# Kernel optimization log

Hardware: AMD Instinct MI355X
Metric: run time of the kernel (lower is better)

## Reference

```python
import jax, jax.numpy as jnp
from jax import lax
import numpy as np

N, M, P, K = 2, 16384, 5023, 4
C_PLANE, HP = 32, 256
OUT_DIM = 32


def _harmonic(x):
    # pytorch3d HarmonicEmbedding(n=4, logspace, omega_0=1, append_input=True)
    f = jnp.asarray([1.0, 2.0, 4.0, 8.0], x.dtype)
    e = (x[..., None] * f).reshape(x.shape[:-1] + (-1,))  # [..., 12]
    return jnp.concatenate([jnp.sin(e), jnp.cos(e), x], axis=-1)  # [..., 27]


def _grid_sample2d(img, grid):
    # img [C,H,W], grid [M,2] (x->W, y->H) in [-1,1]; bilinear, zero pad, align_corners=False
    C, H, W = img.shape
    x = (grid[:, 0] + 1.0) * (W / 2.0) - 0.5
    y = (grid[:, 1] + 1.0) * (H / 2.0) - 0.5
    x0 = jnp.floor(x); y0 = jnp.floor(y)
    x1 = x0 + 1.0; y1 = y0 + 1.0
    wx1 = x - x0; wx0 = 1.0 - wx1
    wy1 = y - y0; wy0 = 1.0 - wy1
    def gather(ix, iy):
        valid = ((ix >= 0) & (ix < W) & (iy >= 0) & (iy < H)).astype(img.dtype)
        ixc = jnp.clip(ix, 0, W - 1).astype(jnp.int32)
        iyc = jnp.clip(iy, 0, H - 1).astype(jnp.int32)
        return img[:, iyc, ixc] * valid[None, :]  # [C,M]
    out = (gather(x0, y0) * (wx0 * wy0) + gather(x1, y0) * (wx1 * wy0)
           + gather(x0, y1) * (wx0 * wy1) + gather(x1, y1) * (wx1 * wy1))
    return out.T  # [M,C]


def _forward(coordinates, directions, points_position, tex_tplanes, emb_table,
             pw1, pb1, pw2, pb2, fw1, fb1, fw2, fb2, fw3, fb3, dw, db, rw1, rb1, rw2, rb2):
    c = coordinates
    p = points_position
    # --- triplane sampling (EG3D projections (x,y),(x,z),(z,x)), mean over planes ---
    proj = jnp.stack([c[..., :2],
                      c[..., jnp.array([0, 2])],
                      c[..., jnp.array([2, 0])]], axis=1)  # [N,3,M,2]
    tex = jax.vmap(jax.vmap(_grid_sample2d))(tex_tplanes, proj).mean(axis=1)  # [N,M,32]
    # --- KNN (squared distances, ascending, as pytorch3d knn_points) ---
    d2 = (jnp.sum(c * c, -1)[:, :, None] + jnp.sum(p * p, -1)[:, None, :]
          - 2.0 * jnp.einsum('nmc,npc->nmp', c, p))  # [N,M,P]
    negd, idx = lax.top_k(-d2, K)
    dist = -negd  # [N,M,K]
    nn = jax.vmap(lambda pts, i: pts[i])(p, idx)  # [N,M,K,3]
    pf = emb_table[idx]  # [N,M,K,32]
    rel = c[:, :, None, :] - nn
    rel = rel / jnp.maximum(jnp.linalg.norm(rel, axis=-1, keepdims=True), 1e-12)
    h = jnp.concatenate([pf, _harmonic(rel)], axis=-1)  # [N,M,K,59]
    h = jax.nn.relu(h @ pw1 + pb1) @ pw2 + pb2  # [N,M,K,32]
    w = 1.0 / dist
    w = w / jnp.sum(w, axis=1, keepdims=True)  # dim=1 exactly as in source
    pts_feat = jnp.sum(h * w[..., None], axis=2)  # [N,M,32]
    # --- dense MLP stack ---
    feat = jnp.concatenate([tex, pts_feat], axis=-1)  # [N,M,64]
    feat = jax.nn.relu(feat @ fw1 + fb1)
    feat = jax.nn.relu(feat @ fw2 + fb2)
    feat = feat @ fw3 + fb3  # [N,M,128]
    selector = jnp.all((c > -1.0) & (c < 1.0), axis=-1)  # [N,M]
    raw = (jax.nn.softplus(10.0 * (feat @ dw + db)) / 10.0) * selector[..., None]
    densities = 1.0 - jnp.exp(-raw)
    rays = directions / jnp.maximum(jnp.linalg.norm(directions, axis=-1, keepdims=True), 1e-12)
    rgb = jnp.concatenate([feat, _harmonic(rays)], axis=-1)  # [N,M,155]
    rgb = jax.nn.relu(rgb @ rw1 + rb1) @ rw2 + rb2  # [N,M,OUT_DIM]
    rgb = jnp.concatenate([jax.nn.sigmoid(rgb[..., :3]) * (1.0 + 2 * 0.001) - 0.001,
                           rgb[..., 3:]], axis=-1)
    return densities, rgb, dist


def setup_inputs() -> dict:
    key = jax.random.key(0)
    ks = jax.random.split(key, 16)
    rn = lambda k, s, sc=1.0: jax.random.normal(k, s, jnp.float32) * sc
    def lin(k, i, o):
        k1, k2 = jax.random.split(k)
        return rn(k1, (i, o), 1.0 / np.sqrt(i)), rn(k2, (o,), 0.01)
    coordinates = jax.random.uniform(ks[0], (N, M, 3), jnp.float32)
    directions = rn(ks[1], (N, M, 3))
    points_position = jax.random.uniform(ks[2], (N, P, 3), jnp.float32)
    tex_tplanes = rn(ks[3], (N, 3, C_PLANE, HP, HP))
    emb_table = rn(ks[4], (P, 32), 0.02)
    pw1, pb1 = lin(ks[5], 32 + 27, 64)
    pw2, pb2 = lin(ks[6], 64, 32)
    fw1, fb1 = lin(ks[7], 64, 128)
    fw2, fb2 = lin(ks[8], 128, 128)
    fw3, fb3 = lin(ks[9], 128, 128)
    dw, db = lin(ks[10], 128, 1)
    rw1, rb1 = lin(ks[11], 128 + 27, 64)
    rw2, rb2 = lin(ks[12], 64, OUT_DIM)
    return dict(coordinates=coordinates, directions=directions, points_position=points_position,
                tex_tplanes=tex_tplanes, emb_table=emb_table, pw1=pw1, pb1=pb1, pw2=pw2, pb2=pb2,
                fw1=fw1, fb1=fb1, fw2=fw2, fb2=fb2, fw3=fw3, fb3=fb3, dw=dw, db=db,
                rw1=rw1, rb1=rb1, rw2=rw2, rb2=rb2)


def reference(coordinates, directions, points_position, tex_tplanes, emb_table,
              pw1, pb1, pw2, pb2, fw1, fb1, fw2, fb2, fw3, fb3, dw, db, rw1, rb1, rw2, rb2):
    return _forward(coordinates, directions, points_position, tex_tplanes, emb_table,
                    pw1, pb1, pw2, pb2, fw1, fb1, fw2, fb2, fw3, fb3, dw, db, rw1, rb1, rw2, rb2)
```

## Files before the change

### kernel.cpp

```cpp
#include <hip/hip_runtime.h>
#include <float.h>
#include <math.h>

#define NB 2
#define MQ 16384
#define NQ (NB*MQ)
#define PP 5023
#define KNN 4
#define HPX 256
#define HWSZ (HPX*HPX)
#define GD 12
#define GC (GD*GD*GD)
#define CAND_MAX 1024

#define OUT_RGB_OFF  ((size_t)NQ)
#define OUT_DIST_OFF ((size_t)NQ + (size_t)NQ*32)

#define WS_SUMS_OFF   ((size_t)0x80000)
#define WS_PCNT_OFF   ((size_t)0x81000)
#define WS_PSTART_OFF ((size_t)0x85000)
#define WS_PCUR_OFF   ((size_t)0x89000)
#define WS_QCNT_OFF   ((size_t)0x8D000)
#define WS_QSTART_OFF ((size_t)0x91000)
#define WS_QCUR_OFF   ((size_t)0x95000)
#define WS_QID_OFF    ((size_t)0x99000)
#define WS_PG_OFF     ((size_t)0xC0000)
#define WS_PID_OFF    ((size_t)0xF0000)
#define WS_WP_OFF     ((size_t)0x100000)
#define WS_TEX_OFF    ((size_t)0x120000)

#define WP_PW1 0
#define WP_PW2 1920
#define WP_FW1 2944
#define WP_FW2 7040
#define WP_FW3 15232
#define WP_DW  23424
#define WP_RW1 23488
#define WP_RW2 28480

typedef __attribute__((ext_vector_type(2))) _Float16 half2v;

static __device__ __forceinline__ unsigned int pk2(float a, float b) {
    half2v h; h[0] = (_Float16)a; h[1] = (_Float16)b;
    return __builtin_bit_cast(unsigned int, h);
}
static __device__ __forceinline__ float2 upk(unsigned int u) {
    half2v h = __builtin_bit_cast(half2v, u);
    return make_float2((float)h[0], (float)h[1]);
}
static __device__ __forceinline__ float dot2(unsigned int a, unsigned int b, float c) {
    return __builtin_amdgcn_fdot2(__builtin_bit_cast(half2v, a),
                                  __builtin_bit_cast(half2v, b), c, false);
}
static __device__ __forceinline__ int cell_of(float x) {
    int g = (int)(x * (float)GD);
    return (g < 0) ? 0 : ((g > GD-1) ? GD-1 : g);
}

struct FusedArgs {
    const float* src[8];
    int off[8]; int din[8]; int dout[8];
};
__global__ __launch_bounds__(256) void k_fused(
    FusedArgs a, unsigned int* __restrict__ wp,
    const float* __restrict__ tex, unsigned int* __restrict__ tex16,
    const float* __restrict__ pts, const float* __restrict__ coords,
    unsigned int* __restrict__ pcnt, unsigned int* __restrict__ qcnt,
    int use_t)
{
    const int b = blockIdx.x;
    const int tid = threadIdx.x;
    if (b < 1536) {
        if (!use_t) return;
        const int n3 = b >> 8;
        const int hw = ((b & 255) << 8) + tid;
        const float* s = tex + (size_t)n3 * 32 * HWSZ + hw;
        float v[32];
#pragma unroll
        for (int c = 0; c < 32; ++c) v[c] = s[(size_t)c * HWSZ];
        uint4* d = (uint4*)(tex16 + ((size_t)n3 * HWSZ + hw) * 16);
#pragma unroll
        for (int c = 0; c < 4; ++c)
            d[c] = make_uint4(pk2(v[8*c], v[8*c+1]), pk2(v[8*c+2], v[8*c+3]),
                              pk2(v[8*c+4], v[8*c+5]), pk2(v[8*c+6], v[8*c+7]));
    } else if (b < 1536 + 256) {
        const int b2 = b - 1536;
        const int mid = b2 >> 5;
        const int idx = (b2 & 31) * 256 + tid;
        const int DIN = a.din[mid], DOUT = a.dout[mid];
        const int din2 = (DIN + 1) >> 1;
        if (idx >= din2 * DOUT) return;
        const int i2 = idx / DOUT, j = idx - i2 * DOUT;
        const float* s = a.src[mid];
        const float lo = s[(2*i2) * DOUT + j];
        const float hi = (2*i2 + 1 < DIN) ? s[(2*i2 + 1) * DOUT + j] : 0.f;
        wp[a.off[mid] + idx] = pk2(lo, hi);
    } else {
        const int i = (b - 1792) * 256 + tid;
        if (i < NB * PP) {
            const int n = (i >= PP) ? 1 : 0;
            const float px = pts[3*i], py = pts[3*i+1], pz = pts[3*i+2];
            const int c = (cell_of(pz)*GD + cell_of(py))*GD + cell_of(px);
            atomicAdd(&pcnt[n*GC + c], 1u);
        } else if (i - NB*PP < NQ) {
            const int q = i - NB*PP;
            const int n = q >> 14;
            const float cx = coords[3*q], cy = coords[3*q+1], cz = coords[3*q+2];
            const int c = (cell_of(cz)*GD + cell_of(cy))*GD + cell_of(cx);
            atomicAdd(&qcnt[n*GC + c], 1u);
        }
    }
}

__global__ __launch_bounds__(1024) void k_scan2(const unsigned int* __restrict__ pcnt,
                                                unsigned int* __restrict__ psta,
                                                unsigned int* __restrict__ pcur,
                                                const unsigned int* __restrict__ qcnt,
                                                unsigned int* __restrict__ qsta,
                                                unsigned int* __restrict__ qcur) {
    __shared__ unsigned int sc[1024];
    const int t = threadIdx.x;
#pragma unroll 1
    for (int which = 0; which < 2; ++which) {
        const unsigned int* cnt = which ? qcnt : pcnt;
        unsigned int* start  = which ? qsta : psta;
        unsigned int* cursor = which ? qcur : pcur;
        const int stride = which ? MQ : PP;
#pragma unroll 1
        for (int n = 0; n < 2; ++n) {
            const unsigned int* c = cnt + n*GC;
            unsigned int a = (2*t   < GC) ? c[2*t]   : 0u;
            unsigned int b = (2*t+1 < GC) ? c[2*t+1] : 0u;
            unsigned int s = a + b;
            sc[t] = s;
            __syncthreads();
            for (int off = 1; off < 1024; off <<= 1) {
                unsigned int v = (t >= off) ? sc[t - off] : 0u;
                __syncthreads();
                sc[t] += v;
                __syncthreads();
            }
            unsigned int excl = sc[t] - s;
            unsigned int base = n * stride;
            if (2*t < GC)   { start[n*GC + 2*t]   = base + excl;
                              cursor[n*GC + 2*t]  = base + excl; }
            if (2*t+1 < GC) { start[n*GC + 2*t+1] = base + excl + a;
                              cursor[n*GC + 2*t+1]= base + excl + a; }
            __syncthreads();
        }
    }
}

__global__ __launch_bounds__(256) void k_scatter(const float* __restrict__ pts,
                                                 const float* __restrict__ coords,
                                                 unsigned int* __restrict__ pcur,
                                                 unsigned int* __restrict__ qcur,
                                                 float4* __restrict__ pg,
                                                 int* __restrict__ pid,
                                                 int* __restrict__ qid) {
    const int i = blockIdx.x * 256 + threadIdx.x;
    if (i < NB * PP) {
        const int n = (i >= PP) ? 1 : 0;
        const int local = i - n * PP;
        const float px = pts[3*i], py = pts[3*i+1], pz = pts[3*i+2];
        const int c = (cell_of(pz)*GD + cell_of(py))*GD + cell_of(px);
        const unsigned int pos = atomicAdd(&pcur[n*GC + c], 1u);
        pg[pos] = make_float4(px, py, pz, fmaf(px, px, fmaf(py, py, pz*pz)));
        pid[pos] = local;
    } else if (i - NB*PP < NQ) {
        const int q = i - NB*PP;
        const int n = q >> 14;
        const float cx = coords[3*q], cy = coords[3*q+1], cz = coords[3*q+2];
        const int c = (cell_of(cz)*GD + cell_of(cy))*GD + cell_of(cx);
        const unsigned int pos = atomicAdd(&qcur[n*GC + c], 1u);
        qid[pos] = q;
    }
}

__global__ __launch_bounds__(256) void k_knn_cell(
    const float* __restrict__ coords,
    const unsigned int* __restrict__ pstart, const unsigned int* __restrict__ pcnt,
    const float4* __restrict__ pg, const int* __restrict__ pid,
    const unsigned int* __restrict__ qstart, const unsigned int* __restrict__ qcnt,
    const int* __restrict__ qid,
    float* __restrict__ odist, int* __restrict__ oidx)
{
    __shared__ float4 cand[CAND_MAX];
    __shared__ int    cidx[CAND_MAX];
    __shared__ unsigned int rs[25], ro[26];
    const int tid = threadIdx.x;
    const int bid = blockIdx.x;
    const int n = bid / GC, c = bid % GC;
    const unsigned int qn = qcnt[n*GC + c];
    if (qn == 0) return;
    const int gz = c / (GD*GD), gy = (c / GD) % GD, gx = c % GD;

    const int x0 = max(gx-2,0), x1 = min(gx+2,GD-1);
    const int y0 = max(gy-2,0), y1 = min(gy+2,GD-1), ny = y1-y0+1;
    const int z0 = max(gz-2,0), z1 = min(gz+2,GD-1), nz = z1-z0+1;
    const int nrow = ny*nz;

    __shared__ unsigned int rcnt[25];
    if (tid < nrow) {
        const int yy = y0 + tid % ny;
        const int zz = z0 + tid / ny;
        const int c0 = n*GC + (zz*GD + yy)*GD + x0;
        const int c1 = n*GC + (zz*GD + yy)*GD + x1;
        const unsigned int s = pstart[c0];
        rs[tid]   = s;
        rcnt[tid] = (pstart[c1] + pcnt[c1]) - s;
    }
    __syncthreads();
    if (tid == 0) {
        unsigned int acc = 0; ro[0] = 0;
        for (int t = 0; t < nrow; ++t) { acc += rcnt[t]; ro[t+1] = acc; }
    }
    __syncthreads();
    const unsigned int total = ro[nrow];
    const bool ovf = (total > CAND_MAX);
    if (!ovf) {
        for (unsigned int i = tid; i < total; i += 256) {
            int lo = 0, hi = nrow;
            while (hi - lo > 1) { int mid = (lo + hi) >> 1; if (ro[mid] <= i) lo = mid; else hi = mid; }
            const unsigned int src = rs[lo] + (i - ro[lo]);
            cand[i] = pg[src];
            cidx[i] = pid[src];
        }
    }
    __syncthreads();

    const float w = 1.0f / (float)GD;
    const float thresh = 4.f * w * w * 0.999f;
    const int grp = tid >> 4, l16 = tid & 15;
    const unsigned int qs = qstart[n*GC + c];

#define INS4(d, i) { \
        bool L3 = ((d) < bd3) || ((d) == bd3 && (i) < bi3); \
        bool L2 = ((d) < bd2) || ((d) == bd2 && (i) < bi2); \
        bool L1 = ((d) < bd1) || ((d) == bd1 && (i) < bi1); \
        bool L0 = ((d) < bd0) || ((d) == bd0 && (i) < bi0); \
        bd3 = L3 ? (L2 ? bd2 : (d)) : bd3;  bi3 = L3 ? (L2 ? bi2 : (i)) : bi3; \
        bd2 = L2 ? (L1 ? bd1 : (d)) : bd2;  bi2 = L2 ? (L1 ? bi1 : (i)) : bi2; \
        bd1 = L1 ? (L0 ? bd0 : (d)) : bd1;  bi1 = L1 ? (L0 ? bi0 : (i)) : bi1; \
        bd0 = L0 ? (d) : bd0;               bi0 = L0 ? (i) : bi0; }

#define MERGE16() { \
        float bd[4] = { bd0, bd1, bd2, bd3 }; \
        int   bi[4] = { bi0, bi1, bi2, bi3 }; \
        for (int mask = 1; mask < 16; mask <<= 1) { \
            float od[4]; int oi[4]; \
            for (int j = 0; j < 4; ++j) { od[j] = __shfl_xor(bd[j], mask); \
                                          oi[j] = __shfl_xor(bi[j], mask); } \
            float e[4]; int ei[4]; \
            for (int j = 0; j < 4; ++j) { \
                float ad = bd[j], xd = od[3-j]; \
                int   ai = bi[j], xi = oi[3-j]; \
                bool ta = (ad < xd) || (ad == xd && ai < xi); \
                e[j] = ta ? ad : xd; ei[j] = ta ? ai : xi; \
            } \
            { bool sw = (e[2] < e[0]) || (e[2] == e[0] && ei[2] < ei[0]); \
              if (sw) { float td=e[0]; e[0]=e[2]; e[2]=td; int ti=ei[0]; ei[0]=ei[2]; ei[2]=ti; } } \
            { bool sw = (e[3] < e[1]) || (e[3] == e[1] && ei[3] < ei[1]); \
              if (sw) { float td=e[1]; e[1]=e[3]; e[3]=td; int ti=ei[1]; ei[1]=ei[3]; ei[3]=ti; } } \
            { bool sw = (e[1] < e[0]) || (e[1] == e[0] && ei[1] < ei[0]); \
              if (sw) { float td=e[0]; e[0]=e[1]; e[1]=td; int ti=ei[0]; ei[0]=ei[1]; ei[1]=ti; } } \
            { bool sw = (e[3] < e[2]) || (e[3] == e[2] && ei[3] < ei[2]); \
              if (sw) { float td=e[2]; e[2]=e[3]; e[3]=td; int ti=ei[2]; ei[2]=ei[3]; ei[3]=ti; } } \
            for (int j = 0; j < 4; ++j) { bd[j] = e[j]; bi[j] = ei[j]; } \
        } \
        bd0 = bd[0]; bd1 = bd[1]; bd2 = bd[2]; bd3 = bd[3]; \
        bi0 = bi[0]; bi1 = bi[1]; bi2 = bi[2]; bi3 = bi[3]; }

#pragma unroll 1
    for (unsigned int qb = 0; qb < qn; qb += 16) {
        const unsigned int qi = qb + grp;
        if (qi >= qn) continue;
        const int q = qid[qs + qi];
        const float cx = coords[3*q], cy = coords[3*q+1], cz = coords[3*q+2];
        const float ccq = fmaf(cx, cx, fmaf(cy, cy, cz*cz));

        float bd0 = FLT_MAX, bd1 = FLT_MAX, bd2 = FLT_MAX, bd3 = FLT_MAX;
        int   bi0 = 0x7fffffff, bi1 = 0x7fffffff, bi2 = 0x7fffffff, bi3 = 0x7fffffff;

        if (!ovf) {
#pragma unroll 1
            for (unsigned int j = l16; j < total; j += 16) {
                const float4 P = cand[j];
                const int i = cidx[j];
                const float dt = fmaf(cx, P.x, fmaf(cy, P.y, cz * P.z));
                const float d = fmaf(-2.0f, dt, ccq + P.w);
                INS4(d, i)
            }
            MERGE16()
        }
        if (ovf || !(bd3 < thresh)) {
            bd0 = bd1 = bd2 = bd3 = FLT_MAX;
            bi0 = bi1 = bi2 = bi3 = 0x7fffffff;
#pragma unroll 1
            for (int j = l16; j < PP; j += 16) {
                const float4 P = pg[n*PP + j];
                const int i = pid[n*PP + j];
                const float dt = fmaf(cx, P.x, fmaf(cy, P.y, cz * P.z));
                const float d = fmaf(-2.0f, dt, ccq + P.w);
                INS4(d, i)
            }
            MERGE16()
        }
        if (l16 == 0) {
            *(float4*)(odist + (size_t)q*4) = make_float4(bd0, bd1, bd2, bd3);
            *(int4*)(oidx + (size_t)q*4)    = make_int4(bi0, bi1, bi2, bi3);
        }
    }
#undef INS4
#undef MERGE16
}

__global__ __launch_bounds__(1024) void k_sums(const float* __restrict__ dist,
                                               float* __restrict__ sums) {
    const int b = blockIdx.x;
    const int n = b >> 2, k = b & 3;
    float s = 0.f;
    for (int m = threadIdx.x; m < MQ; m += 1024)
        s += 1.0f / dist[((size_t)n * MQ + m) * 4 + k];
    __shared__ float red[1024];
    red[threadIdx.x] = s;
    __syncthreads();
    for (int off = 512; off > 0; off >>= 1) {
        if (threadIdx.x < off) red[threadIdx.x] += red[threadIdx.x + off];
        __syncthreads();
    }
    if (threadIdx.x == 0) sums[b] = red[0];
}

static __device__ __forceinline__ float harm_val(int h, float rx, float ry, float rz) {
    if (h >= 27) return 0.f;
    float v;
    if (h < 24) {
        int base = (h < 12) ? h : (h - 12);
        float rv = (base >> 2) == 0 ? rx : ((base >> 2) == 1 ? ry : rz);
        float e = rv * (float)(1 << (base & 3));
        v = (h < 12) ? sinf(e) : cosf(e);
    } else {
        v = (h == 24) ? rx : ((h == 25) ? ry : rz);
    }
    return v;
}

#define SW 128

template<int DIN2, int DOUT, int TILE>
__device__ __forceinline__ void gemv2(const unsigned int* Xp, int lane,
                                      const unsigned int* Wl,
                                      const float* __restrict__ bias, int j0,
                                      float (&aa)[TILE], float (&ab)[TILE]) {
    static_assert(TILE % 4 == 0, "");
#pragma unroll
    for (int u = 0; u < TILE; ++u) { aa[u] = bias[j0 + u]; ab[u] = aa[u]; }
#pragma unroll
    for (int i2 = 0; i2 < DIN2; ++i2) {
        const uint2 xv = *(const uint2*)(Xp + i2 * SW + 2*lane);
        const uint4* wr = (const uint4*)(Wl + i2 * DOUT + j0);
#pragma unroll
        for (int t = 0; t < TILE/4; ++t) {
            const uint4 w4 = wr[t];
            aa[4*t+0] = dot2(xv.x, w4.x, aa[4*t+0]);  ab[4*t+0] = dot2(xv.y, w4.x, ab[4*t+0]);
            aa[4*t+1] = dot2(xv.x, w4.y, aa[4*t+1]);  ab[4*t+1] = dot2(xv.y, w4.y, ab[4*t+1]);
            aa[4*t+2] = dot2(xv.x, w4.z, aa[4*t+2]);  ab[4*t+2] = dot2(xv.y, w4.z, ab[4*t+2]);
            aa[4*t+3] = dot2(xv.x, w4.w, aa[4*t+3]);  ab[4*t+3] = dot2(xv.y, w4.w, ab[4*t+3]);
        }
    }
}

__global__ __launch_bounds__(1024, 1) void k_main(
    const float* __restrict__ coords, const float* __restrict__ dirs,
    const float* __restrict__ pts, const float* __restrict__ tex_raw,
    const unsigned int* __restrict__ tex16, const float* __restrict__ emb,
    const unsigned int* __restrict__ wp,
    const float* __restrict__ pb1, const float* __restrict__ pb2,
    const float* __restrict__ fb1, const float* __restrict__ fb2,
    const float* __restrict__ fb3, const float* __restrict__ db,
    const float* __restrict__ rb1, const float* __restrict__ rb2,
    const int* __restrict__ idxbuf, const float* __restrict__ distbuf,
    const float* __restrict__ sums, float* __restrict__ out, int use_tex_t)
{
    __shared__ unsigned int S[128 * SW];
    __shared__ __align__(16) unsigned int W[16384];
    __shared__ float Rstg[128 * 33];
    const int tid  = threadIdx.x;
    const int lane = tid & 63;
    const int wv   = __builtin_amdgcn_readfirstlane(tid >> 6);
    const int q0   = blockIdx.x * 128;
    const int n    = q0 >> 14;
    const int qa   = q0 + 2*lane;

#define STAGE(dstu4, srcoff, len) { \
        const uint4* s4_ = (const uint4*)(wp + (srcoff)); \
        for (int i_ = tid; i_ < (len)/4; i_ += 1024) ((uint4*)W)[(dstu4) + i_] = s4_[i_]; }

    auto gatherA = [&](int kk) {
#pragma unroll
        for (int s = 0; s < 2; ++s) {
            const int q = qa + s;
            const int id = idxbuf[(size_t)q*4 + kk];
            if (wv < 8) {
                const float4 e = *(const float4*)(emb + (size_t)id * 32 + wv*4);
                S[(64 + 2*wv    )*SW + 2*lane + s] = pk2(e.x, e.y);
                S[(64 + 2*wv + 1)*SW + 2*lane + s] = pk2(e.z, e.w);
            } else {
                const int w8 = wv - 8;
                if (w8 < 7) {
                    const float cx = coords[q*3+0], cy = coords[q*3+1], cz = coords[q*3+2];
                    const float nx = pts[((size_t)n*PP + id)*3 + 0];
                    const float ny = pts[((size_t)n*PP + id)*3 + 1];
                    const float nz = pts[((size_t)n*PP + id)*3 + 2];
                    float rx = cx - nx, ry = cy - ny, rz = cz - nz;
                    float nrm = sqrtf(fmaf(rx, rx, fmaf(ry, ry, rz*rz)));
                    float inv = 1.f / fmaxf(nrm, 1e-12f);
                    rx *= inv; ry *= inv; rz *= inv;
#pragma unroll
                    for (int t = 0; t < 2; ++t) {
                        const int pr = 2*w8 + t;
                        S[(80 + pr)*SW + 2*lane + s] =
                            pk2(harm_val(2*pr, rx, ry, rz), harm_val(2*pr + 1, rx, ry, rz));
                    }
                }
            }
        }
    };

    unsigned int tex_pack[2];
    {
        const int g = wv;
#pragma unroll
        for (int s = 0; s < 2; ++s) {
            const int q = qa + s;
            const float cx = coords[q*3+0], cy = coords[q*3+1], cz = coords[q*3+2];
            float a0 = 0.f, a1 = 0.f;
#pragma unroll
            for (int pl = 0; pl < 3; ++pl) {
                float gx = (pl == 2) ? cz : cx;
                float gy = (pl == 0) ? cy : ((pl == 1) ? cz : cx);
                float x = (gx + 1.f) * 128.f - 0.5f;
                float y = (gy + 1.f) * 128.f - 0.5f;
                float x0f = floorf(x), y0f = floorf(y);
                float wx1 = x - x0f, wy1 = y - y0f;
                float wx0 = 1.f - wx1, wy0 = 1.f - wy1;
                int x0 = (int)x0f, y0 = (int)y0f;
                int n3 = n * 3 + pl;
                int  xs[4] = { x0, x0+1, x0,   x0+1 };
                int  ys[4] = { y0, y0,   y0+1, y0+1 };
                float wt[4] = { wx0*wy0, wx1*wy0, wx0*wy1, wx1*wy1 };
#pragma unroll
                for (int c = 0; c < 4; ++c) {
                    int xi = xs[c], yi = ys[c];
                    if (xi >= 0 && xi < HPX && yi >= 0 && yi < HPX) {
                        float wgt = wt[c];
                        if (use_tex_t) {
                            const unsigned int v = tex16[
                                ((size_t)n3 * HWSZ + (size_t)yi * HPX + xi) * 16 + g];
                            const float2 f = upk(v);
                            a0 = fmaf(wgt, f.x, a0);
                            a1 = fmaf(wgt, f.y, a1);
                        } else {
                            size_t base = ((size_t)(n3 * 32 + g * 2)) * HWSZ + (size_t)yi * HPX + xi;
                            a0 = fmaf(wgt, tex_raw[base], a0);
                            a1 = fmaf(wgt, tex_raw[base + HWSZ], a1);
                        }
                    }
                }
            }
            tex_pack[s] = pk2(a0 * (1.f/3.f), a1 * (1.f/3.f));
        }
    }

    STAGE(0,    WP_PW1, 1920)
    STAGE(512,  WP_PW2, 1024)
    STAGE(1024, WP_FW1, 4096)
    gatherA(0);
    __syncthreads();

    STAGE(2048, WP_FW2, 8192)

#pragma unroll 1
    for (int k = 0; k < KNN; ++k) {
        {
            float aa[4], ab[4];
            gemv2<30, 64, 4>(S + 64*SW, lane, W, pb1, wv * 4, aa, ab);
            S[(96 + 2*wv    )*SW + 2*lane + 0] = pk2(fmaxf(aa[0], 0.f), fmaxf(aa[1], 0.f));
            S[(96 + 2*wv    )*SW + 2*lane + 1] = pk2(fmaxf(ab[0], 0.f), fmaxf(ab[1], 0.f));
            S[(96 + 2*wv + 1)*SW + 2*lane + 0] = pk2(fmaxf(aa[2], 0.f), fmaxf(aa[3], 0.f));
            S[(96 + 2*wv + 1)*SW + 2*lane + 1] = pk2(fmaxf(ab[2], 0.f), fmaxf(ab[3], 0.f));
        }
        __syncthreads();
        {
            float aa[2], ab[2];
            aa[0] = pb2[wv*2 + 0]; aa[1] = pb2[wv*2 + 1];
            ab[0] = aa[0]; ab[1] = aa[1];
#pragma unroll
            for (int i2 = 0; i2 < 32; ++i2) {
                const uint2 xv = *(const uint2*)(S + (96 + i2)*SW + 2*lane);
                const unsigned int w0 = W[2048 + i2*32 + wv*2 + 0];
                const unsigned int w1 = W[2048 + i2*32 + wv*2 + 1];
                aa[0] = dot2(xv.x, w0, aa[0]);  ab[0] = dot2(xv.y, w0, ab[0]);
                aa[1] = dot2(xv.x, w1, aa[1]);  ab[1] = dot2(xv.y, w1, ab[1]);
            }
            const float da  = distbuf[(size_t)qa*4 + k];
            const float dbq = distbuf[(size_t)(qa+1)*4 + k];
            const float wka = (1.0f / da)  / sums[n*4 + k];
            const float wkb = (1.0f / dbq) / sums[n*4 + k];
            S[(k*16 + wv)*SW + 2*lane + 0] = pk2(wka * aa[0], wka * aa[1]);
            S[(k*16 + wv)*SW + 2*lane + 1] = pk2(wkb * ab[0], wkb * ab[1]);
        }
        if (k < KNN-1) {
            gatherA(k+1);
        } else {
            S[(64 + wv)*SW + 2*lane + 0] = tex_pack[0];
            S[(64 + wv)*SW + 2*lane + 1] = tex_pack[1];
#pragma unroll
            for (int s = 0; s < 2; ++s) {
                float a = 0.f, b = 0.f;
#pragma unroll
                for (int kk = 0; kk < 4; ++kk) {
                    float2 v = upk(S[(kk*16 + wv)*SW + 2*lane + s]);
                    a += v.x; b += v.y;
                }
                S[(80 + wv)*SW + 2*lane + s] = pk2(a, b);
            }
        }
        __syncthreads();
    }

    {
        float aa[8], ab[8];
        gemv2<32, 128, 8>(S + 64*SW, lane, W + 4096, fb1, wv * 8, aa, ab);
#pragma unroll
        for (int u = 0; u < 4; ++u) {
            S[(4*wv + u)*SW + 2*lane + 0] = pk2(fmaxf(aa[2*u], 0.f), fmaxf(aa[2*u+1], 0.f));
            S[(4*wv + u)*SW + 2*lane + 1] = pk2(fmaxf(ab[2*u], 0.f), fmaxf(ab[2*u+1], 0.f));
        }
    }
    __syncthreads();
    {
        float aa[8], ab[8];
        gemv2<64, 128, 8>(S, lane, W + 8192, fb2, wv * 8, aa, ab);
#pragma unroll
        for (int u = 0; u < 4; ++u) {
            S[(64 + 4*wv + u)*SW + 2*lane + 0] = pk2(fmaxf(aa[2*u], 0.f), fmaxf(aa[2*u+1], 0.f));
            S[(64 + 4*wv + u)*SW + 2*lane + 1] = pk2(fmaxf(ab[2*u], 0.f), fmaxf(ab[2*u+1], 0.f));
        }
    }
    STAGE(0, WP_FW3, 8192)
    __syncthreads();
    {
        float aa[8], ab[8];
        gemv2<64, 128, 8>(S + 64*SW, lane, W, fb3, wv * 8, aa, ab);
#pragma unroll
        for (int u = 0; u < 4; ++u) {
            S[(4*wv + u)*SW + 2*lane + 0] = pk2(aa[2*u], aa[2*u+1]);
            S[(4*wv + u)*SW + 2*lane + 1] = pk2(ab[2*u], ab[2*u+1]);
        }
    }
    STAGE(2048, WP_RW1, 4992)
    STAGE(3296, WP_RW2, 1024)
    STAGE(3552, WP_DW, 64)
    __syncthreads();
    if (wv < 14) {
#pragma unroll
        for (int s = 0; s < 2; ++s) {
            const int q = qa + s;
            float dx = dirs[q*3+0], dy = dirs[q*3+1], dz = dirs[q*3+2];
            float dn = sqrtf(fmaf(dx, dx, fmaf(dy, dy, dz*dz)));
            float inv = 1.f / fmaxf(dn, 1e-12f);
            dx *= inv; dy *= inv; dz *= inv;
            S[(64 + wv)*SW + 2*lane + s] = pk2(harm_val(2*wv, dx, dy, dz),
                                               harm_val(2*wv + 1, dx, dy, dz));
        }
    }
    __syncthreads();
    {
        float aa[4], ab[4];
        gemv2<78, 64, 4>(S, lane, W + 8192, rb1, wv * 4, aa, ab);
        S[(78 + 2*wv    )*SW + 2*lane + 0] = pk2(fmaxf(aa[0], 0.f), fmaxf(aa[1], 0.f));
        S[(78 + 2*wv    )*SW + 2*lane + 1] = pk2(fmaxf(ab[0], 0.f), fmaxf(ab[1], 0.f));
        S[(78 + 2*wv + 1)*SW + 2*lane + 0] = pk2(fmaxf(aa[2], 0.f), fmaxf(aa[3], 0.f));
        S[(78 + 2*wv + 1)*SW + 2*lane + 1] = pk2(fmaxf(ab[2], 0.f), fmaxf(ab[3], 0.f));
    }
    __syncthreads();
    {
        float aa[2], ab[2];
        aa[0] = rb2[wv*2 + 0]; aa[1] = rb2[wv*2 + 1];
        ab[0] = aa[0]; ab[1] = aa[1];
#pragma unroll
        for (int i2 = 0; i2 < 32; ++i2) {
            const uint2 xv = *(const uint2*)(S + (78 + i2)*SW + 2*lane);
            const unsigned int w0 = W[13184 + i2*32 + wv*2 + 0];
            const unsigned int w1 = W[13184 + i2*32 + wv*2 + 1];
            aa[0] = dot2(xv.x, w0, aa[0]);  ab[0] = dot2(xv.y, w0, ab[0]);
            aa[1] = dot2(xv.x, w1, aa[1]);  ab[1] = dot2(xv.y, w1, ab[1]);
        }
#pragma unroll
        for (int u = 0; u < 2; ++u) {
            const int j = wv*2 + u;
            float va = (u == 0) ? aa[0] : aa[1];
            float vb = (u == 0) ? ab[0] : ab[1];
            if (j < 3) {
                va = 1.002f * (1.f / (1.f + expf(-va))) - 0.001f;
                vb = 1.002f * (1.f / (1.f + expf(-vb))) - 0.001f;
            }
            Rstg[(2*lane    ) * 33 + j] = va;
            Rstg[(2*lane + 1) * 33 + j] = vb;
        }
        if (wv == 15) {
            float za = db[0], zb = db[0];
#pragma unroll 8
            for (int i2 = 0; i2 < 64; ++i2) {
                const uint2 xv = *(const uint2*)(S + i2*SW + 2*lane);
                const unsigned int wz = W[14208 + i2];
                za = dot2(xv.x, wz, za);
                zb = dot2(xv.y, wz, zb);
            }
#pragma unroll
            for (int s = 0; s < 2; ++s) {
                const int q = qa + s;
                const float z = (s == 0) ? za : zb;
                const float cx = coords[q*3+0], cy = coords[q*3+1], cz = coords[q*3+2];
                float selv = (cx > -1.f && cx < 1.f && cy > -1.f && cy < 1.f &&
                              cz > -1.f && cz < 1.f) ? 1.f : 0.f;
                float t10 = 10.f * z;
                float sp = (t10 > 20.f) ? t10 : log1pf(expf(t10));
                float raw = sp * 0.1f * selv;
                out[q] = 1.f - expf(-raw);
            }
        }
    }
    __syncthreads();
    {
        const int cq = tid >> 3;
        const int j0 = (tid & 7) * 4;
        float4 v;
        v.x = Rstg[cq*33 + j0 + 0];
        v.y = Rstg[cq*33 + j0 + 1];
        v.z = Rstg[cq*33 + j0 + 2];
        v.w = Rstg[cq*33 + j0 + 3];
        *(float4*)(out + OUT_RGB_OFF + ((size_t)(q0 + cq))*32 + j0) = v;
    }
#undef STAGE
}

extern "C" void kernel_launch(void* const* d_in, const int* in_sizes, int n_in,
                              void* d_out, int out_size, void* d_ws, size_t ws_size,
                              hipStream_t stream) {
    (void)in_sizes; (void)n_in; (void)out_size;
    const float* coords = (const float*)d_in[0];
    const float* dirs   = (const float*)d_in[1];
    const float* pts    = (const float*)d_in[2];
    const float* tex    = (const float*)d_in[3];
    const float* emb    = (const float*)d_in[4];
    const float* pw1 = (const float*)d_in[5];  const float* pb1 = (const float*)d_in[6];
    const float* pw2 = (const float*)d_in[7];  const float* pb2 = (const float*)d_in[8];
    const float* fw1 = (const float*)d_in[9];  const float* fb1 = (const float*)d_in[10];
    const float* fw2 = (const float*)d_in[11]; const float* fb2 = (const float*)d_in[12];
    const float* fw3 = (const float*)d_in[13]; const float* fb3 = (const float*)d_in[14];
    const float* dw  = (const float*)d_in[15]; const float* db  = (const float*)d_in[16];
    const float* rw1 = (const float*)d_in[17]; const float* rb1 = (const float*)d_in[18];
    const float* rw2 = (const float*)d_in[19]; const float* rb2 = (const float*)d_in[20];

    float*        out     = (float*)d_out;
    int*          wsidx   = (int*)d_ws;
    float*        wssums  = (float*)((char*)d_ws + WS_SUMS_OFF);
    unsigned int* wspcnt  = (unsigned int*)((char*)d_ws + WS_PCNT_OFF);
    unsigned int* wspsta  = (unsigned int*)((char*)d_ws + WS_PSTART_OFF);
    unsigned int* wspcur  = (unsigned int*)((char*)d_ws + WS_PCUR_OFF);
    unsigned int* wsqcnt  = (unsigned int*)((char*)d_ws + WS_QCNT_OFF);
    unsigned int* wsqsta  = (unsigned int*)((char*)d_ws + WS_QSTART_OFF);
    unsigned int* wsqcur  = (unsigned int*)((char*)d_ws + WS_QCUR_OFF);
    int*          wsqid   = (int*)((char*)d_ws + WS_QID_OFF);
    float4*       wspg    = (float4*)((char*)d_ws + WS_PG_OFF);
    int*          wspid   = (int*)((char*)d_ws + WS_PID_OFF);
    unsigned int* wswp    = (unsigned int*)((char*)d_ws + WS_WP_OFF);
    unsigned int* wstex   = (unsigned int*)((char*)d_ws + WS_TEX_OFF);

    const size_t need_tex = WS_TEX_OFF + (size_t)6 * HWSZ * 16 * 4;
    const int use_t = (ws_size >= need_tex) ? 1 : 0;

    FusedArgs fa;
    fa.src[0] = pw1; fa.off[0] = WP_PW1; fa.din[0] = 59;  fa.dout[0] = 64;
    fa.src[1] = pw2; fa.off[1] = WP_PW2; fa.din[1] = 64;  fa.dout[1] = 32;
    fa.src[2] = fw1; fa.off[2] = WP_FW1; fa.din[2] = 64;  fa.dout[2] = 128;
    fa.src[3] = fw2; fa.off[3] = WP_FW2; fa.din[3] = 128; fa.dout[3] = 128;
    fa.src[4] = fw3; fa.off[4] = WP_FW3; fa.din[4] = 128; fa.dout[4] = 128;
    fa.src[5] = dw;  fa.off[5] = WP_DW;  fa.din[5] = 128; fa.dout[5] = 1;
    fa.src[6] = rw1; fa.off[6] = WP_RW1; fa.din[6] = 155; fa.dout[6] = 64;
    fa.src[7] = rw2; fa.off[7] = WP_RW2; fa.din[7] = 64;  fa.dout[7] = 32;

    const int nitems = NB*PP + NQ;
    const int count_blocks = (nitems + 255) / 256;
    hipMemsetAsync((char*)d_ws + WS_PCNT_OFF, 0, WS_QSTART_OFF - WS_PCNT_OFF, stream);
    k_fused<<<1792 + count_blocks, 256, 0, stream>>>(fa, wswp, tex, wstex,
                                                     pts, coords, wspcnt, wsqcnt, use_t);
    k_scan2<<<1, 1024, 0, stream>>>(wspcnt, wspsta, wspcur, wsqcnt, wsqsta, wsqcur);
    k_scatter<<<count_blocks, 256, 0, stream>>>(pts, coords, wspcur, wsqcur,
                                                wspg, wspid, wsqid);
    k_knn_cell<<<NB*GC, 256, 0, stream>>>(coords, wspsta, wspcnt, wspg, wspid,
                                          wsqsta, wsqcnt, wsqid,
                                          out + OUT_DIST_OFF, wsidx);
    k_sums<<<8, 1024, 0, stream>>>(out + OUT_DIST_OFF, wssums);
    k_main<<<NQ / 128, 1024, 0, stream>>>(coords, dirs, pts, tex, wstex, emb,
                                          wswp, pb1, pb2, fb1, fb2, fb3, db, rb1, rb2,
                                          wsidx, out + OUT_DIST_OFF, wssums, out, use_t);
}
```

Baseline: 273.4 us.

## Fuse inverse-distance sums into KNN kernel and use wave-shuffle scan

Removes the separate k_sums launch by having each KNN block accumulate per-k inverse-distance partial sums and add them atomically into 64-bit fixed-point counters, which k_main converts back to float. Fixed-point integer atomics keep the sum deterministic regardless of block order. The single-block prefix scan now uses wavefront shuffles plus a small cross-wave scan instead of a barrier-heavy shared-memory Hillis-Steele loop. Trade-offs: fixed-point quantisation and possible overflow if inverse distances are very large (tiny distances), plus one extra atomic per block.

```diff
diff --git a/kernel.cpp b/kernel.cpp
--- a/kernel.cpp
+++ b/kernel.cpp
@@ -12,6 +12,7 @@
 #define GD 12
 #define GC (GD*GD*GD)
 #define CAND_MAX 1024
+#define SUM_SCALE 16384.f
 
 #define OUT_RGB_OFF  ((size_t)NQ)
 #define OUT_DIST_OFF ((size_t)NQ + (size_t)NQ*32)
@@ -118,8 +119,9 @@
                                                 const unsigned int* __restrict__ qcnt,
                                                 unsigned int* __restrict__ qsta,
                                                 unsigned int* __restrict__ qcur) {
-    __shared__ unsigned int sc[1024];
+    __shared__ unsigned int wsum[16];
     const int t = threadIdx.x;
+    const int lane = t & 63, wv = t >> 6;
 #pragma unroll 1
     for (int which = 0; which < 2; ++which) {
         const unsigned int* cnt = which ? qcnt : pcnt;
@@ -132,16 +134,27 @@
             unsigned int a = (2*t   < GC) ? c[2*t]   : 0u;
             unsigned int b = (2*t+1 < GC) ? c[2*t+1] : 0u;
             unsigned int s = a + b;
-            sc[t] = s;
+            unsigned int inc = s;
+#pragma unroll
+            for (int off = 1; off < 64; off <<= 1) {
+                unsigned int v = __shfl_up(inc, off);
+                if (lane >= off) inc += v;
+            }
+            if (lane == 63) wsum[wv] = inc;
             __syncthreads();
-            for (int off = 1; off < 1024; off <<= 1) {
-                unsigned int v = (t >= off) ? sc[t - off] : 0u;
-                __syncthreads();
-                sc[t] += v;
-                __syncthreads();
-            }
-            unsigned int excl = sc[t] - s;
-            unsigned int base = n * stride;
+            if (wv == 0) {
+                unsigned int x = (lane < 16) ? wsum[lane] : 0u;
+                unsigned int xin = x;
+#pragma unroll
+                for (int off = 1; off < 16; off <<= 1) {
+                    unsigned int v = __shfl_up(xin, off);
+                    if (lane >= off) xin += v;
+                }
+                if (lane < 16) wsum[lane] = xin - x;
+            }
+            __syncthreads();
+            const unsigned int excl = wsum[wv] + (inc - s);
+            const unsigned int base = n * stride;
             if (2*t < GC)   { start[n*GC + 2*t]   = base + excl;
                               cursor[n*GC + 2*t]  = base + excl; }
             if (2*t+1 < GC) { start[n*GC + 2*t+1] = base + excl + a;
@@ -183,7 +196,8 @@
     const float4* __restrict__ pg, const int* __restrict__ pid,
     const unsigned int* __restrict__ qstart, const unsigned int* __restrict__ qcnt,
     const int* __restrict__ qid,
-    float* __restrict__ odist, int* __restrict__ oidx)
+    float* __restrict__ odist, int* __restrict__ oidx,
+    unsigned long long* __restrict__ sums64)
 {
     __shared__ float4 cand[CAND_MAX];
     __shared__ int    cidx[CAND_MAX];
@@ -233,6 +247,7 @@
     const float thresh = 4.f * w * w * 0.999f;
     const int grp = tid >> 4, l16 = tid & 15;
     const unsigned int qs = qstart[n*GC + c];
+    float sA0 = 0.f, sA1 = 0.f, sA2 = 0.f, sA3 = 0.f;
 
 #define INS4(d, i) { \
         bool L3 = ((d) < bd3) || ((d) == bd3 && (i) < bi3); \
@@ -309,27 +324,30 @@
         if (l16 == 0) {
             *(float4*)(odist + (size_t)q*4) = make_float4(bd0, bd1, bd2, bd3);
             *(int4*)(oidx + (size_t)q*4)    = make_int4(bi0, bi1, bi2, bi3);
+            sA0 += 1.0f / bd0;  sA1 += 1.0f / bd1;
+            sA2 += 1.0f / bd2;  sA3 += 1.0f / bd3;
         }
     }
 #undef INS4
 #undef MERGE16
-}
-
-__global__ __launch_bounds__(1024) void k_sums(const float* __restrict__ dist,
-                                               float* __restrict__ sums) {
-    const int b = blockIdx.x;
-    const int n = b >> 2, k = b & 3;
-    float s = 0.f;
-    for (int m = threadIdx.x; m < MQ; m += 1024)
-        s += 1.0f / dist[((size_t)n * MQ + m) * 4 + k];
-    __shared__ float red[1024];
-    red[threadIdx.x] = s;
-    __syncthreads();
-    for (int off = 512; off > 0; off >>= 1) {
-        if (threadIdx.x < off) red[threadIdx.x] += red[threadIdx.x + off];
+
+    __syncthreads();
+    {
+        float4* red = cand;
+        if (l16 == 0) red[tid >> 4] = make_float4(sA0, sA1, sA2, sA3);
         __syncthreads();
-    }
-    if (threadIdx.x == 0) sums[b] = red[0];
+        if (tid == 0) {
+            float s0 = 0.f, s1 = 0.f, s2 = 0.f, s3 = 0.f;
+            for (int i = 0; i < 16; ++i) {
+                const float4 v = red[i];
+                s0 += v.x; s1 += v.y; s2 += v.z; s3 += v.w;
+            }
+            atomicAdd(&sums64[n*4 + 0], (unsigned long long)(s0 * SUM_SCALE + 0.5f));
+            atomicAdd(&sums64[n*4 + 1], (unsigned long long)(s1 * SUM_SCALE + 0.5f));
+            atomicAdd(&sums64[n*4 + 2], (unsigned long long)(s2 * SUM_SCALE + 0.5f));
+            atomicAdd(&sums64[n*4 + 3], (unsigned long long)(s3 * SUM_SCALE + 0.5f));
+        }
+    }
 }
 
 static __device__ __forceinline__ float harm_val(int h, float rx, float ry, float rz) {
@@ -381,7 +399,8 @@
     const float* __restrict__ fb3, const float* __restrict__ db,
     const float* __restrict__ rb1, const float* __restrict__ rb2,
     const int* __restrict__ idxbuf, const float* __restrict__ distbuf,
-    const float* __restrict__ sums, float* __restrict__ out, int use_tex_t)
+    const unsigned long long* __restrict__ sums64, float* __restrict__ out,
+    int use_tex_t)
 {
     __shared__ unsigned int S[128 * SW];
     __shared__ __align__(16) unsigned int W[16384];
@@ -504,10 +523,11 @@
                 aa[0] = dot2(xv.x, w0, aa[0]);  ab[0] = dot2(xv.y, w0, ab[0]);
                 aa[1] = dot2(xv.x, w1, aa[1]);  ab[1] = dot2(xv.y, w1, ab[1]);
             }
+            const float fsum = (float)sums64[n*4 + k] * (1.f / SUM_SCALE);
             const float da  = distbuf[(size_t)qa*4 + k];
             const float dbq = distbuf[(size_t)(qa+1)*4 + k];
-            const float wka = (1.0f / da)  / sums[n*4 + k];
-            const float wkb = (1.0f / dbq) / sums[n*4 + k];
+            const float wka = (1.0f / da)  / fsum;
+            const float wkb = (1.0f / dbq) / fsum;
             S[(k*16 + wv)*SW + 2*lane + 0] = pk2(wka * aa[0], wka * aa[1]);
             S[(k*16 + wv)*SW + 2*lane + 1] = pk2(wkb * ab[0], wkb * ab[1]);
         }
@@ -667,7 +687,7 @@
 
     float*        out     = (float*)d_out;
     int*          wsidx   = (int*)d_ws;
-    float*        wssums  = (float*)((char*)d_ws + WS_SUMS_OFF);
+    unsigned long long* wssums64 = (unsigned long long*)((char*)d_ws + WS_SUMS_OFF);
     unsigned int* wspcnt  = (unsigned int*)((char*)d_ws + WS_PCNT_OFF);
     unsigned int* wspsta  = (unsigned int*)((char*)d_ws + WS_PSTART_OFF);
     unsigned int* wspcur  = (unsigned int*)((char*)d_ws + WS_PCUR_OFF);
@@ -695,7 +715,7 @@
 
     const int nitems = NB*PP + NQ;
     const int count_blocks = (nitems + 255) / 256;
-    hipMemsetAsync((char*)d_ws + WS_PCNT_OFF, 0, WS_QSTART_OFF - WS_PCNT_OFF, stream);
+    hipMemsetAsync((char*)d_ws + WS_SUMS_OFF, 0, WS_QSTART_OFF - WS_SUMS_OFF, stream);
     k_fused<<<1792 + count_blocks, 256, 0, stream>>>(fa, wswp, tex, wstex,
                                                      pts, coords, wspcnt, wsqcnt, use_t);
     k_scan2<<<1, 1024, 0, stream>>>(wspcnt, wspsta, wspcur, wsqcnt, wsqsta, wsqcur);
@@ -703,9 +723,8 @@
                                                 wspg, wspid, wsqid);
     k_knn_cell<<<NB*GC, 256, 0, stream>>>(coords, wspsta, wspcnt, wspg, wspid,
                                           wsqsta, wsqcnt, wsqid,
-                                          out + OUT_DIST_OFF, wsidx);
-    k_sums<<<8, 1024, 0, stream>>>(out + OUT_DIST_OFF, wssums);
+                                          out + OUT_DIST_OFF, wsidx, wssums64);
     k_main<<<NQ / 128, 1024, 0, stream>>>(coords, dirs, pts, tex, wstex, emb,
                                           wswp, pb1, pb2, fb1, fb2, fb3, db, rb1, rb2,
-                                          wsidx, out + OUT_DIST_OFF, wssums, out, use_t);
-}
+                                          wsidx, out + OUT_DIST_OFF, wssums64, out, use_t);
+}
```

After: 412.3 us. 50.8% more time.
